# Kernel optimization log

Hardware: AMD Instinct MI355X
Metric: run time of the kernel (lower is better)

The kernel has to match this reference:

```python
import jax, jax.numpy as jnp
import numpy as np

IN_FEATURES = 4096
OUT_FEATURES = 4096
DENSE_OUT = int(0.85 * OUT_FEATURES)          # 3481
SPARSE_OUT = OUT_FEATURES - DENSE_OUT         # 615


def setup_inputs() -> dict:
    key = jax.random.key(0)
    kx, kw = jax.random.split(key)
    x = jax.random.normal(kx, (4, 2048, IN_FEATURES), dtype=jnp.float32)
    weights = jax.random.normal(kw, (OUT_FEATURES, IN_FEATURES), dtype=jnp.float32)
    return {"x": x, "weights": weights}


def reference(x, weights):
    # Module partitions weight rows: first SPARSE_OUT rows go through sputnik
    # SpMM, the remaining DENSE_OUT rows through a cutlass GEMM, then outputs
    # are concatenated as [sparse, dense] -> identical to x @ weights.T.
    size_out = x.shape[:-1] + (OUT_FEATURES,)
    xf = x.reshape(-1, x.shape[-1])                      # [N, in]
    w_sparse = weights[:SPARSE_OUT, :]                   # [615, in]
    w_dense = weights[SPARSE_OUT:, :]                    # [3481, in]
    out_sparse = jnp.einsum('ni,oi->no', xf, w_sparse)   # SpMM branch
    out_dense = jnp.einsum('ni,oi->no', xf, w_dense)     # GEMM branch
    out = jnp.concatenate([out_sparse, out_dense], axis=1)
    return out.reshape(size_out)
```

## Files before the change

### kernel.cpp

```cpp
#include <hip/hip_runtime.h>
#include <cstdint>
#include <cstddef>

#define K_DIM 4096
#define N_DIM 4096
#define BM 256
#define BN 256
#define BK 64
#define NT (K_DIM / BK)

typedef __attribute__((ext_vector_type(8))) short short8;
typedef __attribute__((ext_vector_type(4))) float floatx4;

__device__ __forceinline__ unsigned pack_bf16x2(float lo, float hi) {
    unsigned ul = __float_as_uint(lo);
    unsigned uh = __float_as_uint(hi);
    ul = (ul + 0x7FFFu + ((ul >> 16) & 1u)) >> 16;
    uh = (uh + 0x7FFFu + ((uh >> 16) & 1u)) & 0xFFFF0000u;
    return (ul & 0xFFFFu) | uh;
}

__global__ __launch_bounds__(256) void cast2_f32_bf16_kernel(
        const float* __restrict__ x, const float* __restrict__ w,
        uint4* __restrict__ a16, uint4* __restrict__ b16,
        long nx, long nw) {
    const long xc = nx >> 3;
    const long total = (nx + nw) >> 3;
    long c = (long)blockIdx.x * 256 + threadIdx.x;
    const long stride = (long)gridDim.x * 256;
    for (; c < total; c += stride) {
        const float4* src;
        uint4* dst;
        if (c < xc) { src = (const float4*)x + (c << 1); dst = a16 + c; }
        else { const long d = c - xc; src = (const float4*)w + (d << 1); dst = b16 + d; }
        const float4 a = src[0];
        const float4 b = src[1];
        uint4 o;
        o.x = pack_bf16x2(a.x, a.y);
        o.y = pack_bf16x2(a.z, a.w);
        o.z = pack_bf16x2(b.x, b.y);
        o.w = pack_bf16x2(b.z, b.w);
        *dst = o;
    }
}

__global__ __launch_bounds__(512, 2) void gemm_bf16_bt(
        const unsigned short* __restrict__ A,
        const unsigned short* __restrict__ B,
        float* __restrict__ C, int M) {
    __shared__ unsigned short sAb[4 * 128 * 64];
    __shared__ unsigned short sBb[4 * 128 * 64];

    const int tid  = threadIdx.x;
    const int lane = tid & 63;
    const int wave = tid >> 6;
    const int wqm  = wave >> 2;
    const int wqn  = wave & 3;
    const int quad = lane >> 4;
    const int l16  = lane & 15;

    const int nbn = N_DIM / BN;
    int wg = blockIdx.x;
    const int cpx = gridDim.x >> 3;
    wg = (wg & 7) * cpx + (wg >> 3);
    const int bm = wg / nbn;
    const int bn = wg % nbn;

    const int srow     = wave * 8 + (lane >> 3);
    const int kblk_src = (lane & 7) ^ ((lane >> 3) & 7);

    const unsigned short* ag = A + ((size_t)bm * BM + srow) * K_DIM + kblk_src * 8;
    const unsigned short* bg = B + ((size_t)bn * BN + srow) * K_DIM + kblk_src * 8;

#define STAGE(gptr, sptr, slot, half, kt)                                        \
    do {                                                                         \
        _Pragma("unroll")                                                        \
        for (int j_ = 0; j_ < 2; ++j_)                                           \
            __builtin_amdgcn_global_load_lds(                                    \
                (const __attribute__((address_space(1))) void*)(                 \
                    (gptr) + (size_t)((half) * 128 + j_ * 64) * K_DIM            \
                           + (size_t)(kt) * BK),                                 \
                (__attribute__((address_space(3))) void*)(                       \
                    (sptr) + (slot) * 8192 + (j_ * 64 + wave * 8) * BK),         \
                16, 0, 0);                                                       \
    } while (0)

    floatx4 acc[2][2][4][2];
#pragma unroll
    for (int a = 0; a < 2; ++a)
#pragma unroll
        for (int b = 0; b < 2; ++b)
#pragma unroll
            for (int c = 0; c < 4; ++c)
#pragma unroll
                for (int d = 0; d < 2; ++d)
                    acc[a][b][c][d] = (floatx4)0.0f;

    short8 af[4][2];
    short8 bf0[2][2];
    short8 bf1[2][2];

#define LDA(slot)                                                                \
    do {                                                                         \
        _Pragma("unroll")                                                        \
        for (int mt_ = 0; mt_ < 4; ++mt_)                                        \
        _Pragma("unroll")                                                        \
        for (int ks_ = 0; ks_ < 2; ++ks_)                                        \
            af[mt_][ks_] = *(const short8*)(sAb + (slot) * 8192 +                \
                (wqm * 64 + mt_ * 16 + l16) * BK +                               \
                ((((ks_ << 2) | quad) ^ (l16 & 7)) << 3));                       \
    } while (0)

#define LDB(dst, slot)                                                           \
    do {                                                                         \
        _Pragma("unroll")                                                        \
        for (int nt_ = 0; nt_ < 2; ++nt_)                                        \
        _Pragma("unroll")                                                        \
        for (int ks_ = 0; ks_ < 2; ++ks_)                                        \
            dst[nt_][ks_] = *(const short8*)(sBb + (slot) * 8192 +               \
                (wqn * 32 + nt_ * 16 + l16) * BK +                               \
                ((((ks_ << 2) | quad) ^ (l16 & 7)) << 3));                       \
    } while (0)

#define MMA(qm, qn, bfv)                                                         \
    do {                                                                         \
        __builtin_amdgcn_s_setprio(1);                                           \
        _Pragma("unroll")                                                        \
        for (int mt_ = 0; mt_ < 4; ++mt_)                                        \
        _Pragma("unroll")                                                        \
        for (int nt_ = 0; nt_ < 2; ++nt_)                                        \
        _Pragma("unroll")                                                        \
        for (int ks_ = 0; ks_ < 2; ++ks_)                                        \
            acc[qm][qn][mt_][nt_] = __builtin_amdgcn_mfma_f32_16x16x32_bf16(     \
                af[mt_][ks_], bfv[nt_][ks_], acc[qm][qn][mt_][nt_], 0, 0, 0);    \
        __builtin_amdgcn_s_setprio(0);                                           \
    } while (0)

#define ENDPHASE(n)                                                              \
    do {                                                                         \
        asm volatile("s_waitcnt vmcnt(" #n ")" ::: "memory");                    \
        __builtin_amdgcn_s_barrier();                                            \
        __builtin_amdgcn_sched_barrier(0);                                       \
    } while (0)

#define TILE(P0, k)                                                              \
    do {                                                                         \
        STAGE(ag, sAb, ((P0) ^ 2) + 1, 1, (k) + 1);                \
        LDA((P0));                                                               \
        LDB(bf0, (P0));                                                          \
        MMA(0, 0, bf0);                                                          \
        ENDPHASE(6);                                                             \
        STAGE(bg, sBb, ((P0) ^ 2) + 1, 1, (k) + 1);                \
        LDB(bf1, (P0) + 1);                                                      \
        MMA(0, 1, bf1);                                                          \
        ENDPHASE(6);                                                             \
        STAGE(ag, sAb, (P0), 0, (k) + 2);                          \
        LDA((P0) + 1);                                                           \
        MMA(1, 0, bf0);                                                          \
        ENDPHASE(6);                                                             \
        STAGE(bg, sBb, (P0), 0, (k) + 2);                          \
        MMA(1, 1, bf1);                                                          \
        ENDPHASE(6);                                                             \
    } while (0)

#define TILE_NOSYNC(P0)                                                          \
    do {                                                                         \
        LDA((P0));     LDB(bf0, (P0)); MMA(0, 0, bf0);                           \
        LDB(bf1, (P0) + 1);            MMA(0, 1, bf1);                           \
        LDA((P0) + 1);                 MMA(1, 0, bf0);                           \
                                       MMA(1, 1, bf1);                           \
    } while (0)

    STAGE(ag, sAb, 0, 0, 0);
    STAGE(bg, sBb, 0, 0, 0);
    STAGE(ag, sAb, 1, 1, 0);
    STAGE(bg, sBb, 1, 1, 0);
    STAGE(ag, sAb, 2, 0, 1);
    STAGE(bg, sBb, 2, 0, 1);
    asm volatile("s_waitcnt vmcnt(8)" ::: "memory");
    __builtin_amdgcn_s_barrier();
    __builtin_amdgcn_sched_barrier(0);

#pragma unroll 1
    for (int k = 0; k < NT - 2; k += 2) {
        TILE(0, k);
        TILE(2, k + 1);
    }

    STAGE(ag, sAb, 3, 1, NT - 1);
    STAGE(bg, sBb, 3, 1, NT - 1);
    asm volatile("s_waitcnt vmcnt(0)" ::: "memory");
    __builtin_amdgcn_s_barrier();
    __builtin_amdgcn_sched_barrier(0);
    TILE_NOSYNC(0);
    TILE_NOSYNC(2);

#pragma unroll
    for (int qm = 0; qm < 2; ++qm)
#pragma unroll
        for (int qn = 0; qn < 2; ++qn)
#pragma unroll
            for (int mt = 0; mt < 4; ++mt)
#pragma unroll
                for (int nt = 0; nt < 2; ++nt) {
                    const int col = bn * BN + qn * 128 + wqn * 32 + nt * 16 + l16;
                    const size_t row0 = (size_t)bm * BM + qm * 128 + wqm * 64
                                      + mt * 16 + quad * 4;
#pragma unroll
                    for (int r = 0; r < 4; ++r)
                        C[(row0 + r) * N_DIM + col] = acc[qm][qn][mt][nt][r];
                }
}

__global__ __launch_bounds__(256) void gemm_naive_f32(
        const float* __restrict__ X, const float* __restrict__ W,
        float* __restrict__ C, long total) {
    long idx = (long)blockIdx.x * 256 + threadIdx.x;
    if (idx >= total) return;
    const long row = idx / N_DIM, col = idx % N_DIM;
    const float* x = X + row * K_DIM;
    const float* w = W + col * K_DIM;
    float s = 0.f;
    for (int k = 0; k < K_DIM; k += 4) {
        floatx4 a = *(const floatx4*)(x + k);
        floatx4 b = *(const floatx4*)(w + k);
        s += a[0] * b[0] + a[1] * b[1] + a[2] * b[2] + a[3] * b[3];
    }
    C[idx] = s;
}

extern "C" void kernel_launch(void* const* d_in, const int* in_sizes, int n_in,
                              void* d_out, int out_size, void* d_ws, size_t ws_size,
                              hipStream_t stream) {
    const float* x = (const float*)d_in[0];
    const float* w = (const float*)d_in[1];
    float* out = (float*)d_out;

    const long nx = (long)in_sizes[0];
    const long nw = (long)in_sizes[1];
    const int  M  = (int)(nx / K_DIM);

    const size_t a_bytes = (size_t)nx * 2;
    const size_t b_bytes = (size_t)nw * 2;

    if (ws_size >= a_bytes + b_bytes && (M % BM) == 0) {
        unsigned short* a16 = (unsigned short*)d_ws;
        unsigned short* b16 = (unsigned short*)((char*)d_ws + a_bytes);
        cast2_f32_bf16_kernel<<<4096, 256, 0, stream>>>(
            x, w, (uint4*)a16, (uint4*)b16, nx, nw);
        const int nwg = (M / BM) * (N_DIM / BN);
        gemm_bf16_bt<<<dim3(nwg), 512, 0, stream>>>(a16, b16, out, M);
    } else {
        const long total = (long)M * N_DIM;
        gemm_naive_f32<<<(int)((total + 255) / 256), 256, 0, stream>>>(x, w, out, total);
    }
}
```

Before: 502.1 us.

## Fuse fp32-to-bf16 conversion into GEMM staging, drop separate cast kernel

Removes the standalone cast kernel and has the GEMM load fp32 tiles of X and W straight into registers, convert them with v_cvt_pk_bf16_f32, and write swizzled bf16 into LDS. This avoids writing and re-reading the bf16 copies of both inputs and saves one kernel launch. In exchange it gives up the asynchronous global_load_lds path, doubles global bytes per tile, adds VGPR pressure for the staged registers, and every workgroup now re-converts the same shared tiles.

```diff
diff --git a/kernel.cpp b/kernel.cpp
--- a/kernel.cpp
+++ b/kernel.cpp
@@ -12,41 +12,17 @@
 typedef __attribute__((ext_vector_type(8))) short short8;
 typedef __attribute__((ext_vector_type(4))) float floatx4;
 
-__device__ __forceinline__ unsigned pack_bf16x2(float lo, float hi) {
-    unsigned ul = __float_as_uint(lo);
-    unsigned uh = __float_as_uint(hi);
-    ul = (ul + 0x7FFFu + ((ul >> 16) & 1u)) >> 16;
-    uh = (uh + 0x7FFFu + ((uh >> 16) & 1u)) & 0xFFFF0000u;
-    return (ul & 0xFFFFu) | uh;
-}
-
-__global__ __launch_bounds__(256) void cast2_f32_bf16_kernel(
-        const float* __restrict__ x, const float* __restrict__ w,
-        uint4* __restrict__ a16, uint4* __restrict__ b16,
-        long nx, long nw) {
-    const long xc = nx >> 3;
-    const long total = (nx + nw) >> 3;
-    long c = (long)blockIdx.x * 256 + threadIdx.x;
-    const long stride = (long)gridDim.x * 256;
-    for (; c < total; c += stride) {
-        const float4* src;
-        uint4* dst;
-        if (c < xc) { src = (const float4*)x + (c << 1); dst = a16 + c; }
-        else { const long d = c - xc; src = (const float4*)w + (d << 1); dst = b16 + d; }
-        const float4 a = src[0];
-        const float4 b = src[1];
-        uint4 o;
-        o.x = pack_bf16x2(a.x, a.y);
-        o.y = pack_bf16x2(a.z, a.w);
-        o.z = pack_bf16x2(b.x, b.y);
-        o.w = pack_bf16x2(b.z, b.w);
-        *dst = o;
-    }
-}
+__device__ __forceinline__ unsigned cvt_pk_bf16(float lo, float hi) {
+    unsigned r;
+    asm("v_cvt_pk_bf16_f32 %0, %1, %2" : "=v"(r) : "v"(lo), "v"(hi));
+    return r;
+}
+
+typedef struct { float4 t0, t1, t2, t3; } StageRegs;
 
 __global__ __launch_bounds__(512, 2) void gemm_bf16_bt(
-        const unsigned short* __restrict__ A,
-        const unsigned short* __restrict__ B,
+        const float* __restrict__ X,
+        const float* __restrict__ W,
         float* __restrict__ C, int M) {
     __shared__ unsigned short sAb[4 * 128 * 64];
     __shared__ unsigned short sBb[4 * 128 * 64];
@@ -66,23 +42,33 @@
     const int bm = wg / nbn;
     const int bn = wg % nbn;
 
-    const int srow     = wave * 8 + (lane >> 3);
-    const int kblk_src = (lane & 7) ^ ((lane >> 3) & 7);
-
-    const unsigned short* ag = A + ((size_t)bm * BM + srow) * K_DIM + kblk_src * 8;
-    const unsigned short* bg = B + ((size_t)bn * BN + srow) * K_DIM + kblk_src * 8;
-
-#define STAGE(gptr, sptr, slot, half, kt)                                        \
-    do {                                                                         \
-        _Pragma("unroll")                                                        \
-        for (int j_ = 0; j_ < 2; ++j_)                                           \
-            __builtin_amdgcn_global_load_lds(                                    \
-                (const __attribute__((address_space(1))) void*)(                 \
-                    (gptr) + (size_t)((half) * 128 + j_ * 64) * K_DIM            \
-                           + (size_t)(kt) * BK),                                 \
-                (__attribute__((address_space(3))) void*)(                       \
-                    (sptr) + (slot) * 8192 + (j_ * 64 + wave * 8) * BK),         \
-                16, 0, 0);                                                       \
+    const int base_r = wave * 4 + (lane >> 4);
+    const float* ax = X + ((size_t)bm * BM + base_r) * K_DIM + (size_t)l16 * 4;
+    const float* bx = W + ((size_t)bn * BN + base_r) * K_DIM + (size_t)l16 * 4;
+    const int wbase = base_r * 64 + (((l16 >> 1) ^ (base_r & 7)) << 3)
+                    + ((l16 & 1) << 2);
+
+#define STAGE_LOAD(R, gsrc, half, kt)                                            \
+    do {                                                                         \
+        const float* g_ = (gsrc) + ((size_t)(half) * 128) * K_DIM                \
+                                 + (size_t)(kt) * BK;                            \
+        (R).t0 = *(const float4*)(g_);                                           \
+        (R).t1 = *(const float4*)(g_ + (size_t)32 * K_DIM);                      \
+        (R).t2 = *(const float4*)(g_ + (size_t)64 * K_DIM);                      \
+        (R).t3 = *(const float4*)(g_ + (size_t)96 * K_DIM);                      \
+    } while (0)
+
+#define STAGE_WRITE(R, sptr, slot)                                               \
+    do {                                                                         \
+        unsigned short* w_ = (sptr) + (slot) * 8192 + wbase;                     \
+        *(uint2*)(w_ +    0) = make_uint2(cvt_pk_bf16((R).t0.x, (R).t0.y),       \
+                                          cvt_pk_bf16((R).t0.z, (R).t0.w));      \
+        *(uint2*)(w_ + 2048) = make_uint2(cvt_pk_bf16((R).t1.x, (R).t1.y),       \
+                                          cvt_pk_bf16((R).t1.z, (R).t1.w));      \
+        *(uint2*)(w_ + 4096) = make_uint2(cvt_pk_bf16((R).t2.x, (R).t2.y),       \
+                                          cvt_pk_bf16((R).t2.z, (R).t2.w));      \
+        *(uint2*)(w_ + 6144) = make_uint2(cvt_pk_bf16((R).t3.x, (R).t3.y),       \
+                                          cvt_pk_bf16((R).t3.z, (R).t3.w));      \
     } while (0)
 
     floatx4 acc[2][2][4][2];
@@ -136,31 +122,39 @@
         __builtin_amdgcn_s_setprio(0);                                           \
     } while (0)
 
-#define ENDPHASE(n)                                                              \
-    do {                                                                         \
-        asm volatile("s_waitcnt vmcnt(" #n ")" ::: "memory");                    \
+#define ENDPHASE()                                                               \
+    do {                                                                         \
+        asm volatile("" ::: "memory");      \
         __builtin_amdgcn_s_barrier();                                            \
         __builtin_amdgcn_sched_barrier(0);                                       \
     } while (0)
 
 #define TILE(P0, k)                                                              \
     do {                                                                         \
-        STAGE(ag, sAb, ((P0) ^ 2) + 1, 1, (k) + 1);                \
-        LDA((P0));                                                               \
-        LDB(bf0, (P0));                                                          \
-        MMA(0, 0, bf0);                                                          \
-        ENDPHASE(6);                                                             \
-        STAGE(bg, sBb, ((P0) ^ 2) + 1, 1, (k) + 1);                \
-        LDB(bf1, (P0) + 1);                                                      \
-        MMA(0, 1, bf1);                                                          \
-        ENDPHASE(6);                                                             \
-        STAGE(ag, sAb, (P0), 0, (k) + 2);                          \
-        LDA((P0) + 1);                                                           \
-        MMA(1, 0, bf0);                                                          \
-        ENDPHASE(6);                                                             \
-        STAGE(bg, sBb, (P0), 0, (k) + 2);                          \
-        MMA(1, 1, bf1);                                                          \
-        ENDPHASE(6);                                                             \
+        { StageRegs r_;                                                          \
+          STAGE_LOAD(r_, ax, 1, (k) + 1);                          \
+          LDA((P0));                                                             \
+          LDB(bf0, (P0));                                                        \
+          MMA(0, 0, bf0);                                                        \
+          STAGE_WRITE(r_, sAb, ((P0) ^ 2) + 1);                                  \
+        } ENDPHASE();                                                            \
+        { StageRegs r_;                                                          \
+          STAGE_LOAD(r_, bx, 1, (k) + 1);                          \
+          LDB(bf1, (P0) + 1);                                                    \
+          MMA(0, 1, bf1);                                                        \
+          STAGE_WRITE(r_, sBb, ((P0) ^ 2) + 1);                                  \
+        } ENDPHASE();                                                            \
+        { StageRegs r_;                                                          \
+          STAGE_LOAD(r_, ax, 0, (k) + 2);                          \
+          LDA((P0) + 1);                                                         \
+          MMA(1, 0, bf0);                                                        \
+          STAGE_WRITE(r_, sAb, (P0));                                            \
+        } ENDPHASE();                                                            \
+        { StageRegs r_;                                                          \
+          STAGE_LOAD(r_, bx, 0, (k) + 2);                          \
+          MMA(1, 1, bf1);                                                        \
+          STAGE_WRITE(r_, sBb, (P0));                                            \
+        } ENDPHASE();                                                            \
     } while (0)
 
 #define TILE_NOSYNC(P0)                                                          \
@@ -171,15 +165,16 @@
                                        MMA(1, 1, bf1);                           \
     } while (0)
 
-    STAGE(ag, sAb, 0, 0, 0);
-    STAGE(bg, sBb, 0, 0, 0);
-    STAGE(ag, sAb, 1, 1, 0);
-    STAGE(bg, sBb, 1, 1, 0);
-    STAGE(ag, sAb, 2, 0, 1);
-    STAGE(bg, sBb, 2, 0, 1);
-    asm volatile("s_waitcnt vmcnt(8)" ::: "memory");
-    __builtin_amdgcn_s_barrier();
-    __builtin_amdgcn_sched_barrier(0);
+    {
+        StageRegs rA, rB;
+        STAGE_LOAD(rA, ax, 0, 0); STAGE_LOAD(rB, bx, 0, 0);
+        STAGE_WRITE(rA, sAb, 0);  STAGE_WRITE(rB, sBb, 0);
+        STAGE_LOAD(rA, ax, 1, 0); STAGE_LOAD(rB, bx, 1, 0);
+        STAGE_WRITE(rA, sAb, 1);  STAGE_WRITE(rB, sBb, 1);
+        STAGE_LOAD(rA, ax, 0, 1); STAGE_LOAD(rB, bx, 0, 1);
+        STAGE_WRITE(rA, sAb, 2);  STAGE_WRITE(rB, sBb, 2);
+    }
+    __syncthreads();
 
 #pragma unroll 1
     for (int k = 0; k < NT - 2; k += 2) {
@@ -187,11 +182,12 @@
         TILE(2, k + 1);
     }
 
-    STAGE(ag, sAb, 3, 1, NT - 1);
-    STAGE(bg, sBb, 3, 1, NT - 1);
-    asm volatile("s_waitcnt vmcnt(0)" ::: "memory");
-    __builtin_amdgcn_s_barrier();
-    __builtin_amdgcn_sched_barrier(0);
+    {
+        StageRegs rA, rB;
+        STAGE_LOAD(rA, ax, 1, NT - 1); STAGE_WRITE(rA, sAb, 3);
+        STAGE_LOAD(rB, bx, 1, NT - 1); STAGE_WRITE(rB, sBb, 3);
+    }
+    __syncthreads();
     TILE_NOSYNC(0);
     TILE_NOSYNC(2);
 
@@ -237,19 +233,11 @@
     float* out = (float*)d_out;
 
     const long nx = (long)in_sizes[0];
-    const long nw = (long)in_sizes[1];
     const int  M  = (int)(nx / K_DIM);
 
-    const size_t a_bytes = (size_t)nx * 2;
-    const size_t b_bytes = (size_t)nw * 2;
-
-    if (ws_size >= a_bytes + b_bytes && (M % BM) == 0) {
-        unsigned short* a16 = (unsigned short*)d_ws;
-        unsigned short* b16 = (unsigned short*)((char*)d_ws + a_bytes);
-        cast2_f32_bf16_kernel<<<4096, 256, 0, stream>>>(
-            x, w, (uint4*)a16, (uint4*)b16, nx, nw);
+    if ((M % BM) == 0) {
         const int nwg = (M / BM) * (N_DIM / BN);
-        gemm_bf16_bt<<<dim3(nwg), 512, 0, stream>>>(a16, b16, out, M);
+        gemm_bf16_bt<<<dim3(nwg), 512, 0, stream>>>(x, w, out, M);
     } else {
         const long total = (long)M * N_DIM;
         gemm_naive_f32<<<(int)((total + 255) / 256), 256, 0, stream>>>(x, w, out, total);
```

Result: slower. 686.1 us (+36.6%).
